# Performance work log

Hardware: AMD Instinct MI355X
Metric: run time of the kernel (lower is better)

## Reference

```python
import jax, jax.numpy as jnp
import numpy as np

B, N, D, OUT = 2048, 118, 64, 64


def setup_inputs() -> dict:
    key = jax.random.key(0)
    ks = jax.random.split(key, 16)
    inp = {}
    inp["e"] = jax.random.normal(ks[0], (B, N, D), jnp.float32)
    inp["f"] = jax.random.normal(ks[1], (B, N, D), jnp.float32)
    inp["k1"] = jax.random.normal(ks[2], (B, N, N), jnp.float32)
    inp["k2"] = jax.random.normal(ks[3], (B, N, N), jnp.float32)
    inp["G_ndiag"] = jax.random.normal(ks[4], (B, N, N), jnp.float32)
    inp["B_ndiag"] = jax.random.normal(ks[5], (B, N, N), jnp.float32)
    # keep diagonal admittances away from 0 so G^2+B^2 is well-conditioned
    inp["G_diag"] = jax.random.uniform(ks[6], (B, N, 1), jnp.float32) + 0.5
    inp["B_diag"] = jax.random.uniform(ks[7], (B, N, 1), jnp.float32) + 0.5
    inp["Pd"] = jax.random.normal(ks[8], (B, N, 1), jnp.float32)
    inp["Qd"] = jax.random.normal(ks[9], (B, N, 1), jnp.float32)
    s_in = 1.0 / np.sqrt(5 * D)
    inp["W1"] = jax.random.normal(ks[10], (5 * D, OUT), jnp.float32) * s_in
    inp["b1"] = jnp.zeros((OUT,), jnp.float32)
    inp["W2"] = jax.random.normal(ks[11], (5 * D, OUT), jnp.float32) * s_in
    inp["b2"] = jnp.zeros((OUT,), jnp.float32)
    s_a = 1.0 / np.sqrt(D)
    inp["wae"] = jax.random.normal(ks[12], (D, 1), jnp.float32) * s_a
    inp["bae"] = jnp.zeros((1,), jnp.float32)
    inp["waf"] = jax.random.normal(ks[13], (D, 1), jnp.float32) * s_a
    inp["baf"] = jnp.zeros((1,), jnp.float32)
    return inp


def _att(x, w, b):
    # mean-pool over nodes (axis -2, keepdims) then linear+sigmoid -> [B,1,1]
    pooled = jnp.mean(x, axis=-2, keepdims=True)
    return jax.nn.sigmoid(pooled @ w + b)


def reference(e, f, k1, k2, G_ndiag, B_ndiag, G_diag, B_diag, Pd, Qd,
              W1, b1, W2, b2, wae, bae, waf, baf):
    base = e * e + f * f + 0.1
    Ge = G_ndiag @ e
    Gf = G_ndiag @ f
    Be = B_ndiag @ e
    Bf = B_ndiag @ f
    alpha = Pd * e / base + Qd * f / base - Ge - Bf
    # NOTE: original code uses bmm(B_ndiag, f) here (not Be) -- kept faithful
    beta = Qd * e / base - Pd * f / base + Gf + Bf
    base_gb = G_diag * G_diag + B_diag * B_diag
    e3 = (alpha * G_diag + beta * B_diag) / base_gb
    f3 = (beta * G_diag - alpha * B_diag) / base_gb
    base1 = Ge - Bf
    base2 = Gf + Be
    ef2 = e * e + f * f
    Pt = Pd - ef2 * G_diag
    Qt = Qd + ef2 * B_diag
    new_e = (Pt * base1 + Qt * base2) / base_gb
    new_f = (Pt * base2 - Qt * base1) / base_gb
    e1 = k1 @ e
    f1 = k1 @ f
    e2 = k2 @ e
    f2 = k2 @ f
    a1 = _att(e3, wae, bae)
    a2 = _att(new_e, wae, bae)
    a3 = _att(e1, wae, bae)
    a4 = _att(e2, wae, bae)
    a_base = a1 + a2 + a3 + a4 + 0.0001
    e_new = jnp.concatenate(
        ((a1 / a_base) * e3, (a2 / a_base) * new_e,
         (a3 / a_base) * e1, (a4 / a_base) * e2, e), axis=2)
    b1a = _att(f3, waf, baf)
    b2a = _att(new_f, waf, baf)
    b3a = _att(f1, waf, baf)
    b4a = _att(f2, waf, baf)
    b_base = b1a + b2a + b3a + b4a + 0.0001
    f_new = jnp.concatenate(
        ((b1a / b_base) * f3, (b2a / b_base) * new_f,
         (b3a / b_base) * f1, (b4a / b_base) * f2, f), axis=2)
    e_out = jax.nn.relu(e_new @ W1 + b1)
    f_out = jax.nn.relu(f_new @ W2 + b2)
    return (e_out, f_out)
```

## Files before the change

kernel.cpp:

```cpp
#include <hip/hip_runtime.h>
#include <stdint.h>

#define NB 118
#define MSZ (118*118)
#define EFT_S 136

typedef _Float16 f16x8 __attribute__((ext_vector_type(8)));
typedef float f32x4 __attribute__((ext_vector_type(4)));

__device__ __forceinline__ f32x4 mfma16(f16x8 a, f16x8 b, f32x4 c) {
    return __builtin_amdgcn_mfma_f32_16x16x32_f16(a, b, c, 0, 0, 0);
}

__global__ void prep_w(const float* __restrict__ W1, const float* __restrict__ W2,
                       _Float16* __restrict__ WP)
{
    int g = blockIdx.x * 256 + threadIdx.x;
    if (g >= 5120) return;
    int wsel = g / 2560;
    int r = g % 2560;
    int t = r >> 8;
    int c = (r >> 6) & 3;
    int l = r & 63;
    const float* W = wsel ? W2 : W1;
    _Float16* dst = WP + wsel * 20480 + r * 8;
#pragma unroll
    for (int j = 0; j < 8; j++) {
        int kk = t * 32 + (l >> 4) * 8 + j;
        int col = c * 16 + (l & 15);
        dst[j] = (_Float16)W[kk * 64 + col];
    }
}

__device__ __forceinline__ void stage1(const float* __restrict__ M,
                                       const _Float16* EFt_, int w, int lane,
                                       f32x4 (&acc)[2][8])
{
    const int l15 = lane & 15, lhi = lane >> 4;
#pragma unroll
    for (int t = 0; t < 4; t++) {
        f16x8 afr[2];
#pragma unroll
        for (int rf = 0; rf < 2; rf++) {
            int row = w * 32 + rf * 16 + l15;
            if (row > 117) row = 117;
            int kb = t * 32 + lhi * 8;
            const float* p = M + row * NB + kb;
            float vv[8];
            if (t < 3) {
#pragma unroll
                for (int pr = 0; pr < 4; pr++) {
                    float2 q = *(const float2*)(p + 2 * pr);
                    vv[2 * pr] = q.x; vv[2 * pr + 1] = q.y;
                }
            } else {
#pragma unroll
                for (int pr = 0; pr < 4; pr++) {
                    int k0 = kb + 2 * pr;
                    if (k0 <= 116) {
                        float2 q = *(const float2*)(p + 2 * pr);
                        vv[2 * pr] = q.x; vv[2 * pr + 1] = q.y;
                    } else { vv[2 * pr] = 0.f; vv[2 * pr + 1] = 0.f; }
                }
            }
            f16x8 uu;
#pragma unroll
            for (int j = 0; j < 8; j++) uu[j] = (_Float16)vv[j];
            afr[rf] = uu;
        }
#pragma unroll
        for (int c = 0; c < 8; c++) {
            f16x8 bfr = *(const f16x8*)&EFt_[(c * 16 + l15) * EFT_S + t * 32 + lhi * 8];
#pragma unroll
            for (int rf = 0; rf < 2; rf++) acc[rf][c] = mfma16(afr[rf], bfr, acc[rf][c]);
        }
    }
}

__device__ __forceinline__ void writeRT(_Float16* RT_, const f32x4 (&src)[2][8],
                                        float sE, float sF, int w, int lane)
{
    const int l15 = lane & 15, lhi = lane >> 4;
#pragma unroll
    for (int rf = 0; rf < 2; rf++)
#pragma unroll
        for (int c = 0; c < 4; c++)
#pragma unroll
            for (int r = 0; r < 4; r++) {
                int row = w * 32 + rf * 16 + lhi * 4 + r;
                RT_[row * EFT_S + c * 16 + l15] = (_Float16)(src[rf][c][r] * sE);
                RT_[row * EFT_S + 64 + c * 16 + l15] = (_Float16)(src[rf][c + 4][r] * sF);
            }
}

__device__ __forceinline__ void s2round(const _Float16* RT_,
                                        const _Float16* __restrict__ W1P,
                                        const _Float16* __restrict__ W2P,
                                        int j, int w, int lane,
                                        f32x4 (&VE)[2][4], f32x4 (&VF)[2][4])
{
    const int l15 = lane & 15, lhi = lane >> 4;
#pragma unroll
    for (int th = 0; th < 2; th++) {
        int t = 2 * j + th;
        f16x8 ae[2], af[2];
#pragma unroll
        for (int rf = 0; rf < 2; rf++) {
            int row = w * 32 + rf * 16 + l15;
            int kk = th * 32 + lhi * 8;
            ae[rf] = *(const f16x8*)&RT_[row * EFT_S + kk];
            af[rf] = *(const f16x8*)&RT_[row * EFT_S + 64 + kk];
        }
#pragma unroll
        for (int c = 0; c < 4; c++) {
            f16x8 bw1 = *(const f16x8*)&W1P[((t * 4 + c) * 64 + lane) * 8];
            f16x8 bw2 = *(const f16x8*)&W2P[((t * 4 + c) * 64 + lane) * 8];
#pragma unroll
            for (int rf = 0; rf < 2; rf++) {
                VE[rf][c] = mfma16(ae[rf], bw1, VE[rf][c]);
                VF[rf][c] = mfma16(af[rf], bw2, VF[rf][c]);
            }
        }
    }
}

__global__ __launch_bounds__(256, 2) void gcn_main(
    const float* __restrict__ E, const float* __restrict__ F,
    const float* __restrict__ K1, const float* __restrict__ K2,
    const float* __restrict__ Gn, const float* __restrict__ Bn,
    const float* __restrict__ Gdg, const float* __restrict__ Bdg,
    const float* __restrict__ Pdg, const float* __restrict__ Qdg,
    const float* __restrict__ b1, const float* __restrict__ b2,
    const float* __restrict__ wae, const float* __restrict__ bae,
    const float* __restrict__ waf, const float* __restrict__ baf,
    const _Float16* __restrict__ W1P, const _Float16* __restrict__ W2P,
    float* __restrict__ outE, float* __restrict__ outF)
{
    __shared__ __align__(16) _Float16 EFt[128 * EFT_S];
    __shared__ __align__(16) _Float16 RT[128 * EFT_S];
    __shared__ float cs[4][64];
    __shared__ float msrc[4][64];
    __shared__ float csk[2][128];
    __shared__ float sPd[128], sQd[128], sGd[128], sBd[128];
    __shared__ float a8[8];
    __shared__ float aScE[4], aScF[4];

    const int b = blockIdx.x;
    const int tid = threadIdx.x;
    const int lane = tid & 63;
    const int w = tid >> 6;
    const int l15 = lane & 15;
    const int lhi = lane >> 4;
    const f32x4 Z4 = {0.f, 0.f, 0.f, 0.f};

    {
        uint4 z; z.x = z.y = z.z = z.w = 0u;
        uint4* p = (uint4*)EFt;
        for (int i = tid; i < 128 * EFT_S * 2 / 16; i += 256) p[i] = z;
        ((float*)cs)[tid] = 0.0f;
    }
    if (tid < NB) {
        sPd[tid] = Pdg[b * NB + tid]; sQd[tid] = Qdg[b * NB + tid];
        sGd[tid] = Gdg[b * NB + tid]; sBd[tid] = Bdg[b * NB + tid];
    } else if (tid < 128) {
        sPd[tid] = 0.f; sQd[tid] = 0.f; sGd[tid] = 1.f; sBd[tid] = 1.f;
    }
    __syncthreads();

    const float* eb = E + (size_t)b * NB * 64;
    const float* fb = F + (size_t)b * NB * 64;
    for (int ch = tid; ch < NB * 16; ch += 256) {
        int row = ch >> 4, dq = ch & 15;
        const float4 v = *(const float4*)(eb + row * 64 + dq * 4);
        const float4 u = *(const float4*)(fb + row * 64 + dq * 4);
        EFt[(dq * 4 + 0) * EFT_S + row] = (_Float16)v.x;
        EFt[(dq * 4 + 1) * EFT_S + row] = (_Float16)v.y;
        EFt[(dq * 4 + 2) * EFT_S + row] = (_Float16)v.z;
        EFt[(dq * 4 + 3) * EFT_S + row] = (_Float16)v.w;
        EFt[(64 + dq * 4 + 0) * EFT_S + row] = (_Float16)u.x;
        EFt[(64 + dq * 4 + 1) * EFT_S + row] = (_Float16)u.y;
        EFt[(64 + dq * 4 + 2) * EFT_S + row] = (_Float16)u.z;
        EFt[(64 + dq * 4 + 3) * EFT_S + row] = (_Float16)u.w;
    }
    __syncthreads();

    f32x4 accG[2][8], accB[2][8];
#pragma unroll
    for (int rf = 0; rf < 2; rf++)
#pragma unroll
        for (int c = 0; c < 8; c++) { accG[rf][c] = Z4; accB[rf][c] = Z4; }
    stage1(Gn + (size_t)b * MSZ, EFt, w, lane, accG);
    stage1(Bn + (size_t)b * MSZ, EFt, w, lane, accB);

#pragma unroll
    for (int c = 0; c < 4; c++) {
        float se3 = 0, sf3 = 0, sne = 0, snf = 0;
#pragma unroll
        for (int rf = 0; rf < 2; rf++) {
#pragma unroll
            for (int r = 0; r < 4; r++) {
                int row = w * 32 + rf * 16 + lhi * 4 + r;
                int d = c * 16 + l15;
                float Ge = accG[rf][c][r], Gf = accG[rf][c + 4][r];
                float Be = accB[rf][c][r], Bf = accB[rf][c + 4][r];
                float ev = (float)EFt[d * EFT_S + row];
                float fv = (float)EFt[(64 + d) * EFT_S + row];
                float pd = sPd[row], qd = sQd[row], gd = sGd[row], bd = sBd[row];
                float ef2 = ev * ev + fv * fv;
                float ib = 1.0f / (ef2 + 0.1f);
                float alpha = (pd * ev + qd * fv) * ib - Ge - Bf;
                float beta  = (qd * ev - pd * fv) * ib + Gf + Bf;
                float ibg = 1.0f / (gd * gd + bd * bd);
                float e3 = (alpha * gd + beta * bd) * ibg;
                float f3 = (beta * gd - alpha * bd) * ibg;
                float bs1 = Ge - Bf, bs2 = Gf + Be;
                float Pt = pd - ef2 * gd, Qt = qd + ef2 * bd;
                float ne = (Pt * bs1 + Qt * bs2) * ibg;
                float nf = (Pt * bs2 - Qt * bs1) * ibg;
                accG[rf][c][r] = e3; accG[rf][c + 4][r] = f3;
                accB[rf][c][r] = ne; accB[rf][c + 4][r] = nf;
                if (row < NB) { se3 += e3; sf3 += f3; sne += ne; snf += nf; }
            }
        }
        se3 += __shfl_xor(se3, 16); se3 += __shfl_xor(se3, 32);
        sf3 += __shfl_xor(sf3, 16); sf3 += __shfl_xor(sf3, 32);
        sne += __shfl_xor(sne, 16); sne += __shfl_xor(sne, 32);
        snf += __shfl_xor(snf, 16); snf += __shfl_xor(snf, 32);
        if (lhi == 0) {
            atomicAdd(&cs[0][c * 16 + l15], se3);
            atomicAdd(&cs[1][c * 16 + l15], sne);
            atomicAdd(&cs[2][c * 16 + l15], sf3);
            atomicAdd(&cs[3][c * 16 + l15], snf);
        }
    }
    __syncthreads();

    if (tid < NB) {
        const float* p = K1 + (size_t)b * MSZ + tid;
        float s = 0;
        for (int r = 0; r < NB; r++) s += p[(size_t)r * NB];
        csk[0][tid] = s;
    } else if (tid < 128) csk[0][tid] = 0.f;
    else if (tid < 128 + NB) {
        const float* p = K2 + (size_t)b * MSZ + (tid - 128);
        float s = 0;
        for (int r = 0; r < NB; r++) s += p[(size_t)r * NB];
        csk[1][tid - 128] = s;
    } else csk[1][tid - 128] = 0.f;
    __syncthreads();

    {
        const float* ck = csk[w >> 1];
        int er = (w & 1) * 64 + lane;
        float s = 0;
        for (int n = 0; n < NB; n++) s += ck[n] * (float)EFt[er * EFT_S + n];
        msrc[w][lane] = s;
    }
    __syncthreads();

    {
        const float* srcE = (w == 0) ? cs[0] : (w == 1) ? cs[1] : (w == 2) ? msrc[0] : msrc[2];
        const float* srcF = (w == 0) ? cs[2] : (w == 1) ? cs[3] : (w == 2) ? msrc[1] : msrc[3];
        float xe = srcE[lane] * wae[lane];
        float xf = srcF[lane] * waf[lane];
#pragma unroll
        for (int m = 1; m < 64; m <<= 1) { xe += __shfl_xor(xe, m); xf += __shfl_xor(xf, m); }
        if (lane == 0) {
            a8[w]     = 1.0f / (1.0f + __expf(-(xe * (1.0f / NB) + bae[0])));
            a8[w + 4] = 1.0f / (1.0f + __expf(-(xf * (1.0f / NB) + baf[0])));
        }
    }
    __syncthreads();
    if (tid == 0) {
        float ebs = a8[0] + a8[1] + a8[2] + a8[3] + 1e-4f;
        float fbs = a8[4] + a8[5] + a8[6] + a8[7] + 1e-4f;
#pragma unroll
        for (int j = 0; j < 4; j++) { aScE[j] = a8[j] / ebs; aScF[j] = a8[4 + j] / fbs; }
    }
    __syncthreads();

    f32x4 VE[2][4], VF[2][4];
#pragma unroll
    for (int rf = 0; rf < 2; rf++)
#pragma unroll
        for (int c = 0; c < 4; c++) { VE[rf][c] = Z4; VF[rf][c] = Z4; }

    writeRT(RT, accG, aScE[0], aScF[0], w, lane);
    __syncthreads();
    s2round(RT, W1P, W2P, 0, w, lane, VE, VF);
    __syncthreads();
    writeRT(RT, accB, aScE[1], aScF[1], w, lane);
    __syncthreads();
    s2round(RT, W1P, W2P, 1, w, lane, VE, VF);
    __syncthreads();

    f32x4 accK[2][8];
#pragma unroll
    for (int rf = 0; rf < 2; rf++)
#pragma unroll
        for (int c = 0; c < 8; c++) accK[rf][c] = Z4;
    stage1(K1 + (size_t)b * MSZ, EFt, w, lane, accK);
    writeRT(RT, accK, aScE[2], aScF[2], w, lane);
    __syncthreads();
    s2round(RT, W1P, W2P, 2, w, lane, VE, VF);
    __syncthreads();

#pragma unroll
    for (int rf = 0; rf < 2; rf++)
#pragma unroll
        for (int c = 0; c < 8; c++) accK[rf][c] = Z4;
    stage1(K2 + (size_t)b * MSZ, EFt, w, lane, accK);
    writeRT(RT, accK, aScE[3], aScF[3], w, lane);
    __syncthreads();
    s2round(RT, W1P, W2P, 3, w, lane, VE, VF);

#pragma unroll
    for (int th = 0; th < 2; th++) {
        int t = 8 + th;
        f16x8 ae[2], af[2];
#pragma unroll
        for (int rf = 0; rf < 2; rf++) {
            int row = w * 32 + rf * 16 + l15;
            int kk = th * 32 + lhi * 8;
            f16x8 ue, uf;
#pragma unroll
            for (int jj = 0; jj < 8; jj++) {
                ue[jj] = EFt[(kk + jj) * EFT_S + row];
                uf[jj] = EFt[(64 + kk + jj) * EFT_S + row];
            }
            ae[rf] = ue; af[rf] = uf;
        }
#pragma unroll
        for (int c = 0; c < 4; c++) {
            f16x8 bw1 = *(const f16x8*)&W1P[((t * 4 + c) * 64 + lane) * 8];
            f16x8 bw2 = *(const f16x8*)&W2P[((t * 4 + c) * 64 + lane) * 8];
#pragma unroll
            for (int rf = 0; rf < 2; rf++) {
                VE[rf][c] = mfma16(ae[rf], bw1, VE[rf][c]);
                VF[rf][c] = mfma16(af[rf], bw2, VF[rf][c]);
            }
        }
    }

#pragma unroll
    for (int c = 0; c < 4; c++) {
        float bb1 = b1[c * 16 + l15];
        float bb2 = b2[c * 16 + l15];
#pragma unroll
        for (int rf = 0; rf < 2; rf++) {
#pragma unroll
            for (int r = 0; r < 4; r++) {
                int row = w * 32 + rf * 16 + lhi * 4 + r;
                if (row < NB) {
                    size_t o = ((size_t)b * NB + row) * 64 + c * 16 + l15;
                    outE[o] = fmaxf(VE[rf][c][r] + bb1, 0.0f);
                    outF[o] = fmaxf(VF[rf][c][r] + bb2, 0.0f);
                }
            }
        }
    }
}

extern "C" void kernel_launch(void* const* d_in, const int* in_sizes, int n_in,
                              void* d_out, int out_size, void* d_ws, size_t ws_size,
                              hipStream_t stream)
{
    (void)in_sizes; (void)n_in; (void)out_size; (void)ws_size;
    const float* E   = (const float*)d_in[0];
    const float* F   = (const float*)d_in[1];
    const float* K1  = (const float*)d_in[2];
    const float* K2  = (const float*)d_in[3];
    const float* Gn  = (const float*)d_in[4];
    const float* Bn  = (const float*)d_in[5];
    const float* Gdg = (const float*)d_in[6];
    const float* Bdg = (const float*)d_in[7];
    const float* Pdg = (const float*)d_in[8];
    const float* Qdg = (const float*)d_in[9];
    const float* W1  = (const float*)d_in[10];
    const float* b1  = (const float*)d_in[11];
    const float* W2  = (const float*)d_in[12];
    const float* b2  = (const float*)d_in[13];
    const float* wae = (const float*)d_in[14];
    const float* bae = (const float*)d_in[15];
    const float* waf = (const float*)d_in[16];
    const float* baf = (const float*)d_in[17];

    _Float16* WP = (_Float16*)d_ws;
    float* outE = (float*)d_out;
    float* outF = outE + (size_t)2048 * NB * 64;

    prep_w<<<20, 256, 0, stream>>>(W1, W2, WP);
    gcn_main<<<2048, 256, 0, stream>>>(E, F, K1, K2, Gn, Bn, Gdg, Bdg, Pdg, Qdg,
                                       b1, b2, wae, bae, waf, baf,
                                       WP, WP + 20480, outE, outF);
}
```

Before: 331.6 us.

## Fuse attention sums into GEMM epilogues and alias shared buffers to cut syncs

Attention pooling sums for the K1/K2 products are now taken from the MFMA accumulators through shuffles and shared atomics. This replaces the separate strided column-sum pass over K1/K2 and its mat-vec. Stage-2 inputs are kept in registers as fp16 so a single shared buffer serves both the transposed E/F tile and the per-warp row tile. Because each warp only touches its own rows, most __syncthreads go away, and the attention scales are computed redundantly per warp. The passthrough E/F operand is reloaded from global memory, and the transpose load is vectorized. The costs are higher register pressure and rounding stage-1 results to fp16 before scaling.

```diff
diff --git a/kernel.cpp b/kernel.cpp
--- a/kernel.cpp
+++ b/kernel.cpp
@@ -3,9 +3,10 @@
 
 #define NB 118
 #define MSZ (118*118)
-#define EFT_S 136
+#define S 136
 
 typedef _Float16 f16x8 __attribute__((ext_vector_type(8)));
+typedef _Float16 f16x4 __attribute__((ext_vector_type(4)));
 typedef float f32x4 __attribute__((ext_vector_type(4)));
 
 __device__ __forceinline__ f32x4 mfma16(f16x8 a, f16x8 b, f32x4 c) {
@@ -33,7 +34,7 @@
 }
 
 __device__ __forceinline__ void stage1(const float* __restrict__ M,
-                                       const _Float16* EFt_, int w, int lane,
+                                       const _Float16* SH_, int w, int lane,
                                        f32x4 (&acc)[2][8])
 {
     const int l15 = lane & 15, lhi = lane >> 4;
@@ -70,17 +71,19 @@
         }
 #pragma unroll
         for (int c = 0; c < 8; c++) {
-            f16x8 bfr = *(const f16x8*)&EFt_[(c * 16 + l15) * EFT_S + t * 32 + lhi * 8];
+            f16x8 bfr = *(const f16x8*)&SH_[(c * 16 + l15) * S + t * 32 + lhi * 8];
 #pragma unroll
             for (int rf = 0; rf < 2; rf++) acc[rf][c] = mfma16(afr[rf], bfr, acc[rf][c]);
         }
     }
 }
 
-__device__ __forceinline__ void writeRT(_Float16* RT_, const f32x4 (&src)[2][8],
+__device__ __forceinline__ void writeRT(_Float16* RT_, const f16x4 (&pE)[2][4],
+                                        const f16x4 (&pF)[2][4],
                                         float sE, float sF, int w, int lane)
 {
     const int l15 = lane & 15, lhi = lane >> 4;
+    const _Float16 hE = (_Float16)sE, hF = (_Float16)sF;
 #pragma unroll
     for (int rf = 0; rf < 2; rf++)
 #pragma unroll
@@ -88,8 +91,8 @@
 #pragma unroll
             for (int r = 0; r < 4; r++) {
                 int row = w * 32 + rf * 16 + lhi * 4 + r;
-                RT_[row * EFT_S + c * 16 + l15] = (_Float16)(src[rf][c][r] * sE);
-                RT_[row * EFT_S + 64 + c * 16 + l15] = (_Float16)(src[rf][c + 4][r] * sF);
+                RT_[row * S + c * 16 + l15]      = pE[rf][c][r] * hE;
+                RT_[row * S + 64 + c * 16 + l15] = pF[rf][c][r] * hF;
             }
 }
 
@@ -108,8 +111,8 @@
         for (int rf = 0; rf < 2; rf++) {
             int row = w * 32 + rf * 16 + l15;
             int kk = th * 32 + lhi * 8;
-            ae[rf] = *(const f16x8*)&RT_[row * EFT_S + kk];
-            af[rf] = *(const f16x8*)&RT_[row * EFT_S + 64 + kk];
+            ae[rf] = *(const f16x8*)&RT_[row * S + kk];
+            af[rf] = *(const f16x8*)&RT_[row * S + 64 + kk];
         }
 #pragma unroll
         for (int c = 0; c < 4; c++) {
@@ -136,14 +139,9 @@
     const _Float16* __restrict__ W1P, const _Float16* __restrict__ W2P,
     float* __restrict__ outE, float* __restrict__ outF)
 {
-    __shared__ __align__(16) _Float16 EFt[128 * EFT_S];
-    __shared__ __align__(16) _Float16 RT[128 * EFT_S];
-    __shared__ float cs[4][64];
-    __shared__ float msrc[4][64];
-    __shared__ float csk[2][128];
+    __shared__ __align__(16) _Float16 SH[128 * S];
+    __shared__ float cs[8][64];
     __shared__ float sPd[128], sQd[128], sGd[128], sBd[128];
-    __shared__ float a8[8];
-    __shared__ float aScE[4], aScF[4];
 
     const int b = blockIdx.x;
     const int tid = threadIdx.x;
@@ -153,11 +151,11 @@
     const int lhi = lane >> 4;
     const f32x4 Z4 = {0.f, 0.f, 0.f, 0.f};
 
-    {
-        uint4 z; z.x = z.y = z.z = z.w = 0u;
-        uint4* p = (uint4*)EFt;
-        for (int i = tid; i < 128 * EFT_S * 2 / 16; i += 256) p[i] = z;
-        ((float*)cs)[tid] = 0.0f;
+    ((float*)cs)[tid] = 0.0f;
+    ((float*)cs)[tid + 256] = 0.0f;
+    if (tid < 128) {
+        f16x8 z8 = {};
+        *(f16x8*)&SH[tid * S + 120] = z8;
     }
     if (tid < NB) {
         sPd[tid] = Pdg[b * NB + tid]; sQd[tid] = Qdg[b * NB + tid];
@@ -165,33 +163,39 @@
     } else if (tid < 128) {
         sPd[tid] = 0.f; sQd[tid] = 0.f; sGd[tid] = 1.f; sBd[tid] = 1.f;
     }
-    __syncthreads();
 
     const float* eb = E + (size_t)b * NB * 64;
     const float* fb = F + (size_t)b * NB * 64;
-    for (int ch = tid; ch < NB * 16; ch += 256) {
-        int row = ch >> 4, dq = ch & 15;
-        const float4 v = *(const float4*)(eb + row * 64 + dq * 4);
-        const float4 u = *(const float4*)(fb + row * 64 + dq * 4);
-        EFt[(dq * 4 + 0) * EFT_S + row] = (_Float16)v.x;
-        EFt[(dq * 4 + 1) * EFT_S + row] = (_Float16)v.y;
-        EFt[(dq * 4 + 2) * EFT_S + row] = (_Float16)v.z;
-        EFt[(dq * 4 + 3) * EFT_S + row] = (_Float16)v.w;
-        EFt[(64 + dq * 4 + 0) * EFT_S + row] = (_Float16)u.x;
-        EFt[(64 + dq * 4 + 1) * EFT_S + row] = (_Float16)u.y;
-        EFt[(64 + dq * 4 + 2) * EFT_S + row] = (_Float16)u.z;
-        EFt[(64 + dq * 4 + 3) * EFT_S + row] = (_Float16)u.w;
+    for (int id = tid; id < 960; id += 256) {
+        int m = id >= 480;
+        int r = id - (m ? 480 : 0);
+        int q = r >> 4;
+        int dq = r & 15;
+        const float* src = m ? fb : eb;
+        int dbase = m ? 64 : 0;
+        f32x4 v0, v1, v2, v3;
+        int row = 4 * q;
+        v0 = *(const f32x4*)(src + (row + 0) * 64 + dq * 4);
+        v1 = *(const f32x4*)(src + (row + 1) * 64 + dq * 4);
+        v2 = (row + 2 < NB) ? *(const f32x4*)(src + (row + 2) * 64 + dq * 4) : Z4;
+        v3 = (row + 3 < NB) ? *(const f32x4*)(src + (row + 3) * 64 + dq * 4) : Z4;
+#pragma unroll
+        for (int j = 0; j < 4; j++) {
+            f16x4 t = { (_Float16)v0[j], (_Float16)v1[j], (_Float16)v2[j], (_Float16)v3[j] };
+            *(f16x4*)&SH[(dbase + dq * 4 + j) * S + 4 * q] = t;
+        }
     }
     __syncthreads();
 
-    f32x4 accG[2][8], accB[2][8];
+    f32x4 accA[2][8], accB_[2][8];
 #pragma unroll
     for (int rf = 0; rf < 2; rf++)
 #pragma unroll
-        for (int c = 0; c < 8; c++) { accG[rf][c] = Z4; accB[rf][c] = Z4; }
-    stage1(Gn + (size_t)b * MSZ, EFt, w, lane, accG);
-    stage1(Bn + (size_t)b * MSZ, EFt, w, lane, accB);
-
+        for (int c = 0; c < 8; c++) { accA[rf][c] = Z4; accB_[rf][c] = Z4; }
+    stage1(Gn + (size_t)b * MSZ, SH, w, lane, accA);
+    stage1(Bn + (size_t)b * MSZ, SH, w, lane, accB_);
+
+    f16x4 p0E[2][4], p0F[2][4], p1E[2][4], p1F[2][4];
 #pragma unroll
     for (int c = 0; c < 4; c++) {
         float se3 = 0, sf3 = 0, sne = 0, snf = 0;
@@ -201,10 +205,10 @@
             for (int r = 0; r < 4; r++) {
                 int row = w * 32 + rf * 16 + lhi * 4 + r;
                 int d = c * 16 + l15;
-                float Ge = accG[rf][c][r], Gf = accG[rf][c + 4][r];
-                float Be = accB[rf][c][r], Bf = accB[rf][c + 4][r];
-                float ev = (float)EFt[d * EFT_S + row];
-                float fv = (float)EFt[(64 + d) * EFT_S + row];
+                float Ge = accA[rf][c][r], Gf = accA[rf][c + 4][r];
+                float Be = accB_[rf][c][r], Bf = accB_[rf][c + 4][r];
+                float ev = (float)SH[d * S + row];
+                float fv = (float)SH[(64 + d) * S + row];
                 float pd = sPd[row], qd = sQd[row], gd = sGd[row], bd = sBd[row];
                 float ef2 = ev * ev + fv * fv;
                 float ib = 1.0f / (ef2 + 0.1f);
@@ -217,8 +221,8 @@
                 float Pt = pd - ef2 * gd, Qt = qd + ef2 * bd;
                 float ne = (Pt * bs1 + Qt * bs2) * ibg;
                 float nf = (Pt * bs2 - Qt * bs1) * ibg;
-                accG[rf][c][r] = e3; accG[rf][c + 4][r] = f3;
-                accB[rf][c][r] = ne; accB[rf][c + 4][r] = nf;
+                p0E[rf][c][r] = (_Float16)e3; p0F[rf][c][r] = (_Float16)f3;
+                p1E[rf][c][r] = (_Float16)ne; p1F[rf][c][r] = (_Float16)nf;
                 if (row < NB) { se3 += e3; sf3 += f3; sne += ne; snf += nf; }
             }
         }
@@ -228,56 +232,85 @@
         snf += __shfl_xor(snf, 16); snf += __shfl_xor(snf, 32);
         if (lhi == 0) {
             atomicAdd(&cs[0][c * 16 + l15], se3);
+            atomicAdd(&cs[4][c * 16 + l15], sf3);
             atomicAdd(&cs[1][c * 16 + l15], sne);
-            atomicAdd(&cs[2][c * 16 + l15], sf3);
-            atomicAdd(&cs[3][c * 16 + l15], snf);
+            atomicAdd(&cs[5][c * 16 + l15], snf);
+        }
+    }
+
+    f16x4 p2E[2][4], p2F[2][4], p3E[2][4], p3F[2][4];
+    {
+        f32x4 accK[2][8];
+#pragma unroll
+        for (int rf = 0; rf < 2; rf++)
+#pragma unroll
+            for (int c = 0; c < 8; c++) accK[rf][c] = Z4;
+        stage1(K1 + (size_t)b * MSZ, SH, w, lane, accK);
+#pragma unroll
+        for (int c = 0; c < 4; c++) {
+            float sE = 0, sF = 0;
+#pragma unroll
+            for (int rf = 0; rf < 2; rf++)
+#pragma unroll
+                for (int r = 0; r < 4; r++) {
+                    int row = w * 32 + rf * 16 + lhi * 4 + r;
+                    float ve = accK[rf][c][r], vf = accK[rf][c + 4][r];
+                    p2E[rf][c][r] = (_Float16)ve; p2F[rf][c][r] = (_Float16)vf;
+                    if (row < NB) { sE += ve; sF += vf; }
+                }
+            sE += __shfl_xor(sE, 16); sE += __shfl_xor(sE, 32);
+            sF += __shfl_xor(sF, 16); sF += __shfl_xor(sF, 32);
+            if (lhi == 0) {
+                atomicAdd(&cs[2][c * 16 + l15], sE);
+                atomicAdd(&cs[6][c * 16 + l15], sF);
+            }
+        }
+#pragma unroll
+        for (int rf = 0; rf < 2; rf++)
+#pragma unroll
+            for (int c = 0; c < 8; c++) accK[rf][c] = Z4;
+        stage1(K2 + (size_t)b * MSZ, SH, w, lane, accK);
+#pragma unroll
+        for (int c = 0; c < 4; c++) {
+            float sE = 0, sF = 0;
+#pragma unroll
+            for (int rf = 0; rf < 2; rf++)
+#pragma unroll
+                for (int r = 0; r < 4; r++) {
+                    int row = w * 32 + rf * 16 + lhi * 4 + r;
+                    float ve = accK[rf][c][r], vf = accK[rf][c + 4][r];
+                    p3E[rf][c][r] = (_Float16)ve; p3F[rf][c][r] = (_Float16)vf;
+                    if (row < NB) { sE += ve; sF += vf; }
+                }
+            sE += __shfl_xor(sE, 16); sE += __shfl_xor(sE, 32);
+            sF += __shfl_xor(sF, 16); sF += __shfl_xor(sF, 32);
+            if (lhi == 0) {
+                atomicAdd(&cs[3][c * 16 + l15], sE);
+                atomicAdd(&cs[7][c * 16 + l15], sF);
+            }
         }
     }
     __syncthreads();
 
-    if (tid < NB) {
-        const float* p = K1 + (size_t)b * MSZ + tid;
-        float s = 0;
-        for (int r = 0; r < NB; r++) s += p[(size_t)r * NB];
-        csk[0][tid] = s;
-    } else if (tid < 128) csk[0][tid] = 0.f;
-    else if (tid < 128 + NB) {
-        const float* p = K2 + (size_t)b * MSZ + (tid - 128);
-        float s = 0;
-        for (int r = 0; r < NB; r++) s += p[(size_t)r * NB];
-        csk[1][tid - 128] = s;
-    } else csk[1][tid - 128] = 0.f;
-    __syncthreads();
-
+    float sEs[4], sFs[4];
     {
-        const float* ck = csk[w >> 1];
-        int er = (w & 1) * 64 + lane;
-        float s = 0;
-        for (int n = 0; n < NB; n++) s += ck[n] * (float)EFt[er * EFT_S + n];
-        msrc[w][lane] = s;
-    }
-    __syncthreads();
-
-    {
-        const float* srcE = (w == 0) ? cs[0] : (w == 1) ? cs[1] : (w == 2) ? msrc[0] : msrc[2];
-        const float* srcF = (w == 0) ? cs[2] : (w == 1) ? cs[3] : (w == 2) ? msrc[1] : msrc[3];
-        float xe = srcE[lane] * wae[lane];
-        float xf = srcF[lane] * waf[lane];
-#pragma unroll
-        for (int m = 1; m < 64; m <<= 1) { xe += __shfl_xor(xe, m); xf += __shfl_xor(xf, m); }
-        if (lane == 0) {
-            a8[w]     = 1.0f / (1.0f + __expf(-(xe * (1.0f / NB) + bae[0])));
-            a8[w + 4] = 1.0f / (1.0f + __expf(-(xf * (1.0f / NB) + baf[0])));
-        }
-    }
-    __syncthreads();
-    if (tid == 0) {
-        float ebs = a8[0] + a8[1] + a8[2] + a8[3] + 1e-4f;
-        float fbs = a8[4] + a8[5] + a8[6] + a8[7] + 1e-4f;
-#pragma unroll
-        for (int j = 0; j < 4; j++) { aScE[j] = a8[j] / ebs; aScF[j] = a8[4 + j] / fbs; }
-    }
-    __syncthreads();
+        float wl_e = wae[lane], wl_f = waf[lane];
+        float b_e = bae[0], b_f = baf[0];
+        float aE[4], aF[4];
+#pragma unroll
+        for (int s2 = 0; s2 < 4; s2++) {
+            float xe = cs[s2][lane] * wl_e;
+            float xf = cs[4 + s2][lane] * wl_f;
+#pragma unroll
+            for (int m = 1; m < 64; m <<= 1) { xe += __shfl_xor(xe, m); xf += __shfl_xor(xf, m); }
+            aE[s2] = 1.0f / (1.0f + __expf(-(xe * (1.0f / NB) + b_e)));
+            aF[s2] = 1.0f / (1.0f + __expf(-(xf * (1.0f / NB) + b_f)));
+        }
+        float ebs = aE[0] + aE[1] + aE[2] + aE[3] + 1e-4f;
+        float fbs = aF[0] + aF[1] + aF[2] + aF[3] + 1e-4f;
+#pragma unroll
+        for (int j = 0; j < 4; j++) { sEs[j] = aE[j] / ebs; sFs[j] = aF[j] / fbs; }
+    }
 
     f32x4 VE[2][4], VF[2][4];
 #pragma unroll
@@ -285,34 +318,14 @@
 #pragma unroll
         for (int c = 0; c < 4; c++) { VE[rf][c] = Z4; VF[rf][c] = Z4; }
 
-    writeRT(RT, accG, aScE[0], aScF[0], w, lane);
-    __syncthreads();
-    s2round(RT, W1P, W2P, 0, w, lane, VE, VF);
-    __syncthreads();
-    writeRT(RT, accB, aScE[1], aScF[1], w, lane);
-    __syncthreads();
-    s2round(RT, W1P, W2P, 1, w, lane, VE, VF);
-    __syncthreads();
-
-    f32x4 accK[2][8];
-#pragma unroll
-    for (int rf = 0; rf < 2; rf++)
-#pragma unroll
-        for (int c = 0; c < 8; c++) accK[rf][c] = Z4;
-    stage1(K1 + (size_t)b * MSZ, EFt, w, lane, accK);
-    writeRT(RT, accK, aScE[2], aScF[2], w, lane);
-    __syncthreads();
-    s2round(RT, W1P, W2P, 2, w, lane, VE, VF);
-    __syncthreads();
-
-#pragma unroll
-    for (int rf = 0; rf < 2; rf++)
-#pragma unroll
-        for (int c = 0; c < 8; c++) accK[rf][c] = Z4;
-    stage1(K2 + (size_t)b * MSZ, EFt, w, lane, accK);
-    writeRT(RT, accK, aScE[3], aScF[3], w, lane);
-    __syncthreads();
-    s2round(RT, W1P, W2P, 3, w, lane, VE, VF);
+    writeRT(SH, p0E, p0F, sEs[0], sFs[0], w, lane);
+    s2round(SH, W1P, W2P, 0, w, lane, VE, VF);
+    writeRT(SH, p1E, p1F, sEs[1], sFs[1], w, lane);
+    s2round(SH, W1P, W2P, 1, w, lane, VE, VF);
+    writeRT(SH, p2E, p2F, sEs[2], sFs[2], w, lane);
+    s2round(SH, W1P, W2P, 2, w, lane, VE, VF);
+    writeRT(SH, p3E, p3F, sEs[3], sFs[3], w, lane);
+    s2round(SH, W1P, W2P, 3, w, lane, VE, VF);
 
 #pragma unroll
     for (int th = 0; th < 2; th++) {
@@ -321,14 +334,18 @@
 #pragma unroll
         for (int rf = 0; rf < 2; rf++) {
             int row = w * 32 + rf * 16 + l15;
-            int kk = th * 32 + lhi * 8;
-            f16x8 ue, uf;
-#pragma unroll
-            for (int jj = 0; jj < 8; jj++) {
-                ue[jj] = EFt[(kk + jj) * EFT_S + row];
-                uf[jj] = EFt[(64 + kk + jj) * EFT_S + row];
-            }
-            ae[rf] = ue; af[rf] = uf;
+            if (row > 117) row = 117;
+            const float* pe = eb + row * 64 + th * 32 + lhi * 8;
+            const float* pf = fb + row * 64 + th * 32 + lhi * 8;
+            f32x4 q0 = *(const f32x4*)pe, q1 = *(const f32x4*)(pe + 4);
+            f32x4 u0 = *(const f32x4*)pf, u1 = *(const f32x4*)(pf + 4);
+            f16x8 te, tf;
+#pragma unroll
+            for (int jj = 0; jj < 4; jj++) {
+                te[jj] = (_Float16)q0[jj]; te[4 + jj] = (_Float16)q1[jj];
+                tf[jj] = (_Float16)u0[jj]; tf[4 + jj] = (_Float16)u1[jj];
+            }
+            ae[rf] = te; af[rf] = tf;
         }
 #pragma unroll
         for (int c = 0; c < 4; c++) {
```

Result: slower. 416.1 us (+25.5%).
